# Performance work log

Measured on AMD Instinct MI355X. Metric: run time of the kernel, lower is better.

## Reference

```python
import jax, jax.numpy as jnp
import numpy as np

NUM_SEQS = 64
NUM_HEADS = 32
NUM_KV_HEADS = 8
HEAD_DIM = 128
BLOCK_SIZE = 16
MAX_SEQLEN_K = 1024
BLOCKS_PER_SEQ = MAX_SEQLEN_K // BLOCK_SIZE  # 64
NUM_BLOCKS = NUM_SEQS * BLOCKS_PER_SEQ      # 4096
SCALE = 1.0 / float(np.sqrt(HEAD_DIM))
EPS = 1e-6
ROPE_BASE = 10000.0


def setup_inputs() -> dict:
    key = jax.random.key(0)
    ks = jax.random.split(key, 8)
    q = jax.random.normal(ks[0], (NUM_SEQS, NUM_HEADS * HEAD_DIM), jnp.float32)
    k = jax.random.normal(ks[1], (NUM_SEQS, NUM_KV_HEADS * HEAD_DIM), jnp.float32)
    v = jax.random.normal(ks[2], (NUM_SEQS, NUM_KV_HEADS * HEAD_DIM), jnp.float32)
    k_cache = jax.random.normal(ks[3], (NUM_BLOCKS, BLOCK_SIZE, NUM_KV_HEADS, HEAD_DIM), jnp.float32)
    v_cache = jax.random.normal(ks[4], (NUM_BLOCKS, BLOCK_SIZE, NUM_KV_HEADS, HEAD_DIM), jnp.float32)
    qw = 1.0 + 0.1 * jax.random.normal(ks[5], (HEAD_DIM,), jnp.float32)
    kw = 1.0 + 0.1 * jax.random.normal(ks[6], (HEAD_DIM,), jnp.float32)
    # neox rotary cos/sin caches over half the head dim
    inv_freq = 1.0 / (ROPE_BASE ** (jnp.arange(0, HEAD_DIM, 2, dtype=jnp.float32) / HEAD_DIM))
    ang = jnp.arange(MAX_SEQLEN_K, dtype=jnp.float32)[:, None] * inv_freq[None, :]  # [S_max, D/2]
    cos_cache = jnp.cos(ang)
    sin_cache = jnp.sin(ang)
    # decode step: each seq has context_lens tokens already; new token at position context_lens-1
    context_lens = jax.random.randint(ks[7], (NUM_SEQS,), MAX_SEQLEN_K // 2, MAX_SEQLEN_K + 1).astype(jnp.int32)
    position = context_lens - 1
    block_tables = jnp.arange(NUM_SEQS * BLOCKS_PER_SEQ, dtype=jnp.int32).reshape(NUM_SEQS, BLOCKS_PER_SEQ)
    slot_mapping = jnp.arange(NUM_SEQS, dtype=jnp.int32) * MAX_SEQLEN_K + position
    return dict(q=q, k=k, v=v, k_cache=k_cache, v_cache=v_cache, qw=qw, kw=kw,
                cos_cache=cos_cache, sin_cache=sin_cache, position=position,
                slot_mapping=slot_mapping, block_tables=block_tables, context_lens=context_lens)


def _rmsnorm(x, w):
    var = jnp.mean(x * x, axis=-1, keepdims=True)
    return x * jax.lax.rsqrt(var + EPS) * w


def _rope_neox(x, cos, sin):
    # x: [..., D]; cos/sin broadcastable to [..., D/2]
    d = x.shape[-1] // 2
    x1, x2 = x[..., :d], x[..., d:]
    return jnp.concatenate([x1 * cos - x2 * sin, x2 * cos + x1 * sin], axis=-1)


def reference(q, k, v, k_cache, v_cache, qw, kw, cos_cache, sin_cache,
              position, slot_mapping, block_tables, context_lens):
    S = q.shape[0]
    q = q.reshape(S, NUM_HEADS, HEAD_DIM)
    k = k.reshape(S, NUM_KV_HEADS, HEAD_DIM)
    v = v.reshape(S, NUM_KV_HEADS, HEAD_DIM)
    # fused qk-norm + rope
    q = _rmsnorm(q, qw)
    k = _rmsnorm(k, kw)
    cos = cos_cache[position][:, None, :]  # [S,1,D/2]
    sin = sin_cache[position][:, None, :]
    q = _rope_neox(q, cos, sin)
    k = _rope_neox(k, cos, sin)
    # reshape_and_cache: scatter new k/v tokens into the paged cache by flat slot index
    kc = k_cache.reshape(-1, NUM_KV_HEADS, HEAD_DIM).at[slot_mapping].set(k)
    vc = v_cache.reshape(-1, NUM_KV_HEADS, HEAD_DIM).at[slot_mapping].set(v)
    kc = kc.reshape(NUM_BLOCKS, BLOCK_SIZE, NUM_KV_HEADS, HEAD_DIM)
    vc = vc.reshape(NUM_BLOCKS, BLOCK_SIZE, NUM_KV_HEADS, HEAD_DIM)
    # paged attention decode: gather each sequence's blocks
    keys = kc[block_tables].reshape(S, MAX_SEQLEN_K, NUM_KV_HEADS, HEAD_DIM)
    vals = vc[block_tables].reshape(S, MAX_SEQLEN_K, NUM_KV_HEADS, HEAD_DIM)
    G = NUM_HEADS // NUM_KV_HEADS
    qg = q.reshape(S, NUM_KV_HEADS, G, HEAD_DIM)
    scores = jnp.einsum('shgd,snhd->shgn', qg, keys) * SCALE  # [S,KVH,G,N]
    valid = jnp.arange(MAX_SEQLEN_K, dtype=jnp.int32)[None, :] < context_lens[:, None]
    scores = jnp.where(valid[:, None, None, :], scores, -jnp.inf)
    probs = jax.nn.softmax(scores, axis=-1)
    out = jnp.einsum('shgn,snhd->shgd', probs, vals)  # [S,KVH,G,D]
    return out.reshape(S, NUM_HEADS * HEAD_DIM)
```

## Files before the change

### kernel.cpp

```cpp
#include <hip/hip_runtime.h>
#include <math.h>

constexpr int kNumSeqs      = 64;
constexpr int kNumHeads     = 32;
constexpr int kNumKVHeads   = 8;
constexpr int kHeadDim      = 128;
constexpr int kGQA          = 4;
constexpr int kKVBlock      = 16;
constexpr int kMaxSeqlen    = 1024;
constexpr int kBlocksPerSeq = 64;
constexpr int kChunk        = 128;
constexpr int kMaxChunks    = kMaxSeqlen / kChunk;
constexpr int kNumSH        = kNumSeqs * kNumKVHeads;
constexpr float kScale      = 0.08838834764831845f;
constexpr float kEps        = 1e-6f;

constexpr size_t kAccElems = (size_t)kNumSH * kMaxChunks * kGQA * kHeadDim;
constexpr size_t kMOff     = kAccElems;
constexpr size_t kLOff     = kAccElems + (size_t)kNumSH * kMaxChunks * kGQA;

__launch_bounds__(256, 4)
__global__ void paged_attn_part(
    const float* __restrict__ q,
    const float* __restrict__ k,
    const float* __restrict__ v,
    const float* __restrict__ k_cache,
    const float* __restrict__ v_cache,
    const float* __restrict__ qw,
    const float* __restrict__ kw,
    const float* __restrict__ cos_cache,
    const float* __restrict__ sin_cache,
    const int*   __restrict__ position,
    const int*   __restrict__ block_tables,
    const int*   __restrict__ context_lens,
    float* __restrict__ ws)
{
  const int item = blockIdx.x;
  const int c    = item >> 9;
  const int sh   = item & (kNumSH - 1);
  const int s    = sh >> 3;
  const int h    = sh & 7;

  const int ctx = context_lens[s];
  const int n0  = c * kChunk;
  if (n0 >= ctx) return;

  const int tid  = threadIdx.x;
  const int wave = tid >> 6;
  const int lane = tid & 63;

  const int pos      = position[s];
  const int cnt      = min(n0 + kChunk, ctx) - n0;
  const int posLocal = pos - n0;
  const bool haspos  = (posLocal >= 0) && (posLocal < cnt);

  float* accw = ws + ((size_t)sh * kMaxChunks + c) * kGQA * kHeadDim;
  float* mw   = ws + kMOff + ((size_t)sh * kMaxChunks + c) * kGQA;
  float* lw   = ws + kLOff + ((size_t)sh * kMaxChunks + c) * kGQA;

  __shared__ __align__(16) float q_lds[kGQA][kHeadDim];
  __shared__ __align__(16) float kn_lds[kHeadDim];
  __shared__ __align__(16) float vn_lds[kHeadDim];
  __shared__ int bt_lds[kChunk / kKVBlock];
  __shared__ __align__(16) float macc[8][kGQA][kHeadDim];
  __shared__ float mm[8][kGQA];
  __shared__ float ml[8][kGQA];

  {
    const int g = wave;
    const float* qrow = q + (size_t)s * (kNumHeads * kHeadDim) + (h * kGQA + g) * kHeadDim;
    float x1 = qrow[lane];
    float x2 = qrow[lane + 64];
    float ss = x1 * x1 + x2 * x2;
    for (int off = 32; off >= 1; off >>= 1) ss += __shfl_xor(ss, off);
    const float r = rsqrtf(ss * (1.0f / kHeadDim) + kEps);
    x1 *= r * qw[lane];
    x2 *= r * qw[lane + 64];
    const float cc  = cos_cache[pos * 64 + lane];
    const float sn  = sin_cache[pos * 64 + lane];
    q_lds[g][lane]      = (x1 * cc - x2 * sn) * kScale;
    q_lds[g][lane + 64] = (x2 * cc + x1 * sn) * kScale;
  }
  if (wave == 0) {
    const float* krow = k + (size_t)s * (kNumKVHeads * kHeadDim) + h * kHeadDim;
    float x1 = krow[lane];
    float x2 = krow[lane + 64];
    float ss = x1 * x1 + x2 * x2;
    for (int off = 32; off >= 1; off >>= 1) ss += __shfl_xor(ss, off);
    const float r = rsqrtf(ss * (1.0f / kHeadDim) + kEps);
    x1 *= r * kw[lane];
    x2 *= r * kw[lane + 64];
    const float cc  = cos_cache[pos * 64 + lane];
    const float sn  = sin_cache[pos * 64 + lane];
    kn_lds[lane]      = x1 * cc - x2 * sn;
    kn_lds[lane + 64] = x2 * cc + x1 * sn;
  } else if (wave == 1) {
    const float* vrow = v + (size_t)s * (kNumKVHeads * kHeadDim) + h * kHeadDim;
    vn_lds[lane]      = vrow[lane];
    vn_lds[lane + 64] = vrow[lane + 64];
  } else if (wave == 2) {
    if (lane < kChunk / kKVBlock)
      bt_lds[lane] = block_tables[s * kBlocksPerSeq + c * (kChunk / kKVBlock) + lane];
  }
  __syncthreads();

  const int half = lane >> 5;
  const int l    = lane & 31;

  float4 qf[kGQA];
  #pragma unroll
  for (int g = 0; g < kGQA; ++g)
    qf[g] = *(const float4*)&q_lds[g][4 * l];

  const int npairs = (cnt + 1) >> 1;

  float mrun[kGQA], lrun[kGQA];
  float4 acc[kGQA];
  #pragma unroll
  for (int g = 0; g < kGQA; ++g) {
    mrun[g] = -3.0e38f; lrun[g] = 0.0f;
    acc[g] = make_float4(0.f, 0.f, 0.f, 0.f);
  }

  for (int b = 0; wave + 16 * b < npairs; ++b) {
    float4 kv[4], vv[4];
    bool   val[4];
    #pragma unroll
    for (int jj = 0; jj < 4; ++jj) {
      const int  p  = wave + 16 * b + 4 * jj;
      const bool pv = (p < npairs);
      const int  pp = pv ? p : (npairs - 1);
      const int  n  = 2 * pp + half;
      val[jj] = pv && (n < cnt);
      const int  nn = (n < cnt) ? n : (cnt - 1);
      const int  blk = bt_lds[nn >> 4];
      const size_t base = (((size_t)blk * kKVBlock + (nn & 15)) * kNumKVHeads + h) * kHeadDim;
      kv[jj] = *(const float4*)(k_cache + base + 4 * l);
      vv[jj] = *(const float4*)(v_cache + base + 4 * l);
      if (haspos && nn == posLocal) {
        kv[jj] = *(const float4*)&kn_lds[4 * l];
        vv[jj] = *(const float4*)&vn_lds[4 * l];
      }
    }

    float sg[4][kGQA];
    #pragma unroll
    for (int jj = 0; jj < 4; ++jj) {
      #pragma unroll
      for (int g = 0; g < kGQA; ++g)
        sg[jj][g] = qf[g].x * kv[jj].x + qf[g].y * kv[jj].y +
                    qf[g].z * kv[jj].z + qf[g].w * kv[jj].w;
    }
    #pragma unroll
    for (int off = 16; off >= 1; off >>= 1) {
      #pragma unroll
      for (int jj = 0; jj < 4; ++jj) {
        #pragma unroll
        for (int g = 0; g < kGQA; ++g) sg[jj][g] += __shfl_xor(sg[jj][g], off);
      }
    }
    #pragma unroll
    for (int jj = 0; jj < 4; ++jj) {
      if (!val[jj]) {
        #pragma unroll
        for (int g = 0; g < kGQA; ++g) sg[jj][g] = -3.0e38f;
      }
    }

    #pragma unroll
    for (int g = 0; g < kGQA; ++g) {
      const float mb = fmaxf(fmaxf(sg[0][g], sg[1][g]), fmaxf(sg[2][g], sg[3][g]));
      const float mn = fmaxf(mrun[g], mb);
      const float f  = __expf(mrun[g] - mn);
      const float p0 = __expf(sg[0][g] - mn);
      const float p1 = __expf(sg[1][g] - mn);
      const float p2 = __expf(sg[2][g] - mn);
      const float p3 = __expf(sg[3][g] - mn);
      lrun[g] = lrun[g] * f + (p0 + p1 + p2 + p3);
      acc[g].x = acc[g].x * f + p0 * vv[0].x + p1 * vv[1].x + p2 * vv[2].x + p3 * vv[3].x;
      acc[g].y = acc[g].y * f + p0 * vv[0].y + p1 * vv[1].y + p2 * vv[2].y + p3 * vv[3].y;
      acc[g].z = acc[g].z * f + p0 * vv[0].z + p1 * vv[1].z + p2 * vv[2].z + p3 * vv[3].z;
      acc[g].w = acc[g].w * f + p0 * vv[0].w + p1 * vv[1].w + p2 * vv[2].w + p3 * vv[3].w;
      mrun[g] = mn;
    }
  }

  {
    const int idx = wave * 2 + half;
    #pragma unroll
    for (int g = 0; g < kGQA; ++g)
      *(float4*)&macc[idx][g][4 * l] = acc[g];
    if (l == 0) {
      #pragma unroll
      for (int g = 0; g < kGQA; ++g) { mm[idx][g] = mrun[g]; ml[idx][g] = lrun[g]; }
    }
  }
  __syncthreads();

  for (int e = tid; e < kGQA * kHeadDim; e += 256) {
    const int g = e >> 7;
    const int d = e & 127;
    float ms = mm[0][g];
    #pragma unroll
    for (int i = 1; i < 8; ++i) ms = fmaxf(ms, mm[i][g]);
    float ls = 0.0f, o = 0.0f;
    #pragma unroll
    for (int i = 0; i < 8; ++i) {
      const float w = __expf(mm[i][g] - ms);
      ls += w * ml[i][g];
      o  += w * macc[i][g][d];
    }
    accw[e] = o;
    if (d == 0) { mw[g] = ms; lw[g] = ls; }
  }
}

__launch_bounds__(128)
__global__ void paged_attn_reduce(const float* __restrict__ ws,
                                  const int* __restrict__ context_lens,
                                  float* __restrict__ out)
{
  const int idx = blockIdx.x;
  const int g   = idx & 3;
  const int sh  = idx >> 2;
  const int d   = threadIdx.x;
  const int s   = sh >> 3;
  const int h   = sh & 7;

  const int nch = (context_lens[s] + kChunk - 1) / kChunk;

  const float* mw = ws + kMOff + (size_t)sh * (kMaxChunks * kGQA);
  const float* lw = ws + kLOff + (size_t)sh * (kMaxChunks * kGQA);

  float mstar = -3.0e38f;
  for (int p = 0; p < nch; ++p) mstar = fmaxf(mstar, mw[p * kGQA + g]);

  float lstar = 0.0f, o = 0.0f;
  for (int p = 0; p < nch; ++p) {
    const float w = __expf(mw[p * kGQA + g] - mstar);
    lstar += w * lw[p * kGQA + g];
    const float* accp = ws + ((size_t)sh * kMaxChunks + p) * kGQA * kHeadDim + (size_t)g * kHeadDim;
    o += w * accp[d];
  }
  out[(size_t)s * (kNumHeads * kHeadDim) + (h * kGQA + g) * kHeadDim + d] = o / lstar;
}

extern "C" void kernel_launch(void* const* d_in, const int* in_sizes, int n_in,
                              void* d_out, int out_size, void* d_ws, size_t ws_size,
                              hipStream_t stream) {
  const float* q            = (const float*)d_in[0];
  const float* k            = (const float*)d_in[1];
  const float* v            = (const float*)d_in[2];
  const float* k_cache      = (const float*)d_in[3];
  const float* v_cache      = (const float*)d_in[4];
  const float* qw           = (const float*)d_in[5];
  const float* kw           = (const float*)d_in[6];
  const float* cosc         = (const float*)d_in[7];
  const float* sinc         = (const float*)d_in[8];
  const int*   position     = (const int*)d_in[9];
  const int*   block_tables = (const int*)d_in[11];
  const int*   context_lens = (const int*)d_in[12];
  float* out                = (float*)d_out;
  float* ws                 = (float*)d_ws;

  hipLaunchKernelGGL(paged_attn_part, dim3(kMaxChunks * kNumSH), dim3(256), 0, stream,
                     q, k, v, k_cache, v_cache, qw, kw, cosc, sinc,
                     position, block_tables, context_lens, ws);
  hipLaunchKernelGGL(paged_attn_reduce, dim3(kNumSH * kGQA), dim3(kHeadDim), 0, stream,
                     ws, context_lens, out);
}
```

Measured before the change: 94.41 us.

## Map each half-wave to a KV head so one block covers all heads per token

Each block now handles one sequence and a 64-token chunk across all 8 KV heads. Each half-wave owns one KV head and walks every token in the chunk, so a token's K/V rows for all heads (4 KB contiguous) are read together as coalesced loads. The in-block LDS merge of per-wave partials goes away, and each half-wave writes its own partial to the workspace. The trade-off is a serial 64-token loop per half-wave with less parallel memory-level concurrency per head, and more chunks for the reduce kernel to merge.

```diff
diff --git a/kernel.cpp b/kernel.cpp
--- a/kernel.cpp
+++ b/kernel.cpp
@@ -9,7 +9,7 @@
 constexpr int kKVBlock      = 16;
 constexpr int kMaxSeqlen    = 1024;
 constexpr int kBlocksPerSeq = 64;
-constexpr int kChunk        = 128;
+constexpr int kChunk        = 64;
 constexpr int kMaxChunks    = kMaxSeqlen / kChunk;
 constexpr int kNumSH        = kNumSeqs * kNumKVHeads;
 constexpr float kScale      = 0.08838834764831845f;
@@ -36,10 +36,8 @@
     float* __restrict__ ws)
 {
   const int item = blockIdx.x;
-  const int c    = item >> 9;
-  const int sh   = item & (kNumSH - 1);
-  const int s    = sh >> 3;
-  const int h    = sh & 7;
+  const int c    = item >> 6;
+  const int s    = item & 63;
 
   const int ctx = context_lens[s];
   const int n0  = c * kChunk;
@@ -48,71 +46,69 @@
   const int tid  = threadIdx.x;
   const int wave = tid >> 6;
   const int lane = tid & 63;
+  const int half = lane >> 5;
+  const int j    = lane & 31;
+  const int hh   = wave * 2 + half;
 
   const int pos      = position[s];
   const int cnt      = min(n0 + kChunk, ctx) - n0;
   const int posLocal = pos - n0;
   const bool haspos  = (posLocal >= 0) && (posLocal < cnt);
 
-  float* accw = ws + ((size_t)sh * kMaxChunks + c) * kGQA * kHeadDim;
-  float* mw   = ws + kMOff + ((size_t)sh * kMaxChunks + c) * kGQA;
-  float* lw   = ws + kLOff + ((size_t)sh * kMaxChunks + c) * kGQA;
-
-  __shared__ __align__(16) float q_lds[kGQA][kHeadDim];
-  __shared__ __align__(16) float kn_lds[kHeadDim];
-  __shared__ __align__(16) float vn_lds[kHeadDim];
+  __shared__ __align__(16) float q_lds[kNumHeads][kHeadDim];
+  __shared__ __align__(16) float kn_lds[kNumKVHeads][kHeadDim];
+  __shared__ __align__(16) float vn_lds[kNumKVHeads][kHeadDim];
   __shared__ int bt_lds[kChunk / kKVBlock];
-  __shared__ __align__(16) float macc[8][kGQA][kHeadDim];
-  __shared__ float mm[8][kGQA];
-  __shared__ float ml[8][kGQA];
+
+  const float c0 = cos_cache[pos * 64 + j];
+  const float c1 = cos_cache[pos * 64 + 32 + j];
+  const float s0 = sin_cache[pos * 64 + j];
+  const float s1 = sin_cache[pos * 64 + 32 + j];
 
   {
-    const int g = wave;
-    const float* qrow = q + (size_t)s * (kNumHeads * kHeadDim) + (h * kGQA + g) * kHeadDim;
-    float x1 = qrow[lane];
-    float x2 = qrow[lane + 64];
-    float ss = x1 * x1 + x2 * x2;
-    for (int off = 32; off >= 1; off >>= 1) ss += __shfl_xor(ss, off);
+    const float w0 = qw[j], w1 = qw[j + 32], w2 = qw[j + 64], w3 = qw[j + 96];
+    #pragma unroll
+    for (int g = 0; g < kGQA; ++g) {
+      const int qh = hh * kGQA + g;
+      const float* qrow = q + (size_t)s * (kNumHeads * kHeadDim) + qh * kHeadDim;
+      float x0 = qrow[j], x1 = qrow[j + 32], x2 = qrow[j + 64], x3 = qrow[j + 96];
+      float ss = x0 * x0 + x1 * x1 + x2 * x2 + x3 * x3;
+      #pragma unroll
+      for (int off = 16; off >= 1; off >>= 1) ss += __shfl_xor(ss, off);
+      const float r = rsqrtf(ss * (1.0f / kHeadDim) + kEps);
+      x0 *= r * w0; x1 *= r * w1; x2 *= r * w2; x3 *= r * w3;
+      q_lds[qh][j]      = (x0 * c0 - x2 * s0) * kScale;
+      q_lds[qh][j + 32] = (x1 * c1 - x3 * s1) * kScale;
+      q_lds[qh][j + 64] = (x2 * c0 + x0 * s0) * kScale;
+      q_lds[qh][j + 96] = (x3 * c1 + x1 * s1) * kScale;
+    }
+  }
+  if (haspos) {
+    const float w0 = kw[j], w1 = kw[j + 32], w2 = kw[j + 64], w3 = kw[j + 96];
+    const float* krow = k + (size_t)s * (kNumKVHeads * kHeadDim) + hh * kHeadDim;
+    float x0 = krow[j], x1 = krow[j + 32], x2 = krow[j + 64], x3 = krow[j + 96];
+    float ss = x0 * x0 + x1 * x1 + x2 * x2 + x3 * x3;
+    #pragma unroll
+    for (int off = 16; off >= 1; off >>= 1) ss += __shfl_xor(ss, off);
     const float r = rsqrtf(ss * (1.0f / kHeadDim) + kEps);
-    x1 *= r * qw[lane];
-    x2 *= r * qw[lane + 64];
-    const float cc  = cos_cache[pos * 64 + lane];
-    const float sn  = sin_cache[pos * 64 + lane];
-    q_lds[g][lane]      = (x1 * cc - x2 * sn) * kScale;
-    q_lds[g][lane + 64] = (x2 * cc + x1 * sn) * kScale;
-  }
-  if (wave == 0) {
-    const float* krow = k + (size_t)s * (kNumKVHeads * kHeadDim) + h * kHeadDim;
-    float x1 = krow[lane];
-    float x2 = krow[lane + 64];
-    float ss = x1 * x1 + x2 * x2;
-    for (int off = 32; off >= 1; off >>= 1) ss += __shfl_xor(ss, off);
-    const float r = rsqrtf(ss * (1.0f / kHeadDim) + kEps);
-    x1 *= r * kw[lane];
-    x2 *= r * kw[lane + 64];
-    const float cc  = cos_cache[pos * 64 + lane];
-    const float sn  = sin_cache[pos * 64 + lane];
-    kn_lds[lane]      = x1 * cc - x2 * sn;
-    kn_lds[lane + 64] = x2 * cc + x1 * sn;
-  } else if (wave == 1) {
-    const float* vrow = v + (size_t)s * (kNumKVHeads * kHeadDim) + h * kHeadDim;
-    vn_lds[lane]      = vrow[lane];
-    vn_lds[lane + 64] = vrow[lane + 64];
-  } else if (wave == 2) {
-    if (lane < kChunk / kKVBlock)
-      bt_lds[lane] = block_tables[s * kBlocksPerSeq + c * (kChunk / kKVBlock) + lane];
-  }
+    x0 *= r * w0; x1 *= r * w1; x2 *= r * w2; x3 *= r * w3;
+    kn_lds[hh][j]      = x0 * c0 - x2 * s0;
+    kn_lds[hh][j + 32] = x1 * c1 - x3 * s1;
+    kn_lds[hh][j + 64] = x2 * c0 + x0 * s0;
+    kn_lds[hh][j + 96] = x3 * c1 + x1 * s1;
+    const float* vrow = v + (size_t)s * (kNumKVHeads * kHeadDim) + hh * kHeadDim;
+    *(float4*)&vn_lds[hh][4 * j] = *(const float4*)(vrow + 4 * j);
+  }
+  if (tid < kChunk / kKVBlock)
+    bt_lds[tid] = block_tables[s * kBlocksPerSeq + c * (kChunk / kKVBlock) + tid];
   __syncthreads();
-
-  const int half = lane >> 5;
-  const int l    = lane & 31;
 
   float4 qf[kGQA];
   #pragma unroll
   for (int g = 0; g < kGQA; ++g)
-    qf[g] = *(const float4*)&q_lds[g][4 * l];
-
-  const int npairs = (cnt + 1) >> 1;
+    qf[g] = *(const float4*)&q_lds[hh * kGQA + g][4 * j];
+  const float4 knf = *(const float4*)&kn_lds[hh][4 * j];
+  const float4 vnf = *(const float4*)&vn_lds[hh][4 * j];
 
   float mrun[kGQA], lrun[kGQA];
   float4 acc[kGQA];
@@ -122,25 +118,27 @@
     acc[g] = make_float4(0.f, 0.f, 0.f, 0.f);
   }
 
-  for (int b = 0; wave + 16 * b < npairs; ++b) {
+  const int nb = (cnt + 3) >> 2;
+  for (int b = 0; b < nb; ++b) {
     float4 kv[4], vv[4];
     bool   val[4];
-    #pragma unroll
-    for (int jj = 0; jj < 4; ++jj) {
-      const int  p  = wave + 16 * b + 4 * jj;
-      const bool pv = (p < npairs);
-      const int  pp = pv ? p : (npairs - 1);
-      const int  n  = 2 * pp + half;
-      val[jj] = pv && (n < cnt);
-      const int  nn = (n < cnt) ? n : (cnt - 1);
-      const int  blk = bt_lds[nn >> 4];
-      const size_t base = (((size_t)blk * kKVBlock + (nn & 15)) * kNumKVHeads + h) * kHeadDim;
-      kv[jj] = *(const float4*)(k_cache + base + 4 * l);
-      vv[jj] = *(const float4*)(v_cache + base + 4 * l);
-      if (haspos && nn == posLocal) {
-        kv[jj] = *(const float4*)&kn_lds[4 * l];
-        vv[jj] = *(const float4*)&vn_lds[4 * l];
-      }
+    int    pp4[4];
+    #pragma unroll
+    for (int jj = 0; jj < 4; ++jj) {
+      const int p = 4 * b + jj;
+      val[jj] = (p < cnt);
+      const int pp = val[jj] ? p : (cnt - 1);
+      pp4[jj] = pp;
+      const int blk = bt_lds[pp >> 4];
+      const size_t off =
+          ((size_t)blk * kKVBlock + (pp & 15)) * (kNumKVHeads * kHeadDim) +
+          hh * kHeadDim + 4 * j;
+      kv[jj] = *(const float4*)(k_cache + off);
+      vv[jj] = *(const float4*)(v_cache + off);
+    }
+    #pragma unroll
+    for (int jj = 0; jj < 4; ++jj) {
+      if (haspos && pp4[jj] == posLocal) { kv[jj] = knf; vv[jj] = vnf; }
     }
 
     float sg[4][kGQA];
@@ -185,33 +183,16 @@
     }
   }
 
-  {
-    const int idx = wave * 2 + half;
-    #pragma unroll
-    for (int g = 0; g < kGQA; ++g)
-      *(float4*)&macc[idx][g][4 * l] = acc[g];
-    if (l == 0) {
-      #pragma unroll
-      for (int g = 0; g < kGQA; ++g) { mm[idx][g] = mrun[g]; ml[idx][g] = lrun[g]; }
-    }
-  }
-  __syncthreads();
-
-  for (int e = tid; e < kGQA * kHeadDim; e += 256) {
-    const int g = e >> 7;
-    const int d = e & 127;
-    float ms = mm[0][g];
-    #pragma unroll
-    for (int i = 1; i < 8; ++i) ms = fmaxf(ms, mm[i][g]);
-    float ls = 0.0f, o = 0.0f;
-    #pragma unroll
-    for (int i = 0; i < 8; ++i) {
-      const float w = __expf(mm[i][g] - ms);
-      ls += w * ml[i][g];
-      o  += w * macc[i][g][d];
-    }
-    accw[e] = o;
-    if (d == 0) { mw[g] = ms; lw[g] = ls; }
+  const int sh = s * kNumKVHeads + hh;
+  float* accw = ws + ((size_t)sh * kMaxChunks + c) * (kGQA * kHeadDim);
+  #pragma unroll
+  for (int g = 0; g < kGQA; ++g)
+    *(float4*)(accw + g * kHeadDim + 4 * j) = acc[g];
+  if (j == 0) {
+    float* mw = ws + kMOff + ((size_t)sh * kMaxChunks + c) * kGQA;
+    float* lw = ws + kLOff + ((size_t)sh * kMaxChunks + c) * kGQA;
+    #pragma unroll
+    for (int g = 0; g < kGQA; ++g) { mw[g] = mrun[g]; lw[g] = lrun[g]; }
   }
 }
 
@@ -239,7 +220,8 @@
   for (int p = 0; p < nch; ++p) {
     const float w = __expf(mw[p * kGQA + g] - mstar);
     lstar += w * lw[p * kGQA + g];
-    const float* accp = ws + ((size_t)sh * kMaxChunks + p) * kGQA * kHeadDim + (size_t)g * kHeadDim;
+    const float* accp =
+        ws + ((size_t)sh * kMaxChunks + p) * (kGQA * kHeadDim) + (size_t)g * kHeadDim;
     o += w * accp[d];
   }
   out[(size_t)s * (kNumHeads * kHeadDim) + (h * kGQA + g) * kHeadDim + d] = o / lstar;
@@ -263,7 +245,7 @@
   float* out                = (float*)d_out;
   float* ws                 = (float*)d_ws;
 
-  hipLaunchKernelGGL(paged_attn_part, dim3(kMaxChunks * kNumSH), dim3(256), 0, stream,
+  hipLaunchKernelGGL(paged_attn_part, dim3(kMaxChunks * kNumSeqs), dim3(256), 0, stream,
                      q, k, v, k_cache, v_cache, qw, kw, cosc, sinc,
                      position, block_tables, context_lens, ws);
   hipLaunchKernelGGL(paged_attn_reduce, dim3(kNumSH * kGQA), dim3(kHeadDim), 0, stream,
```

Result: slower. 106.3 us (+12.6%).
